# Performance work log

Hardware: AMD Instinct MI355X
Metric: run time of the kernel (lower is better)

## Reference

```python
import jax, jax.numpy as jnp
import numpy as np

B, S, V, E, H, O = 256, 128, 50000, 256, 512, 32


def _cell(x, h, c, Wih, Whh, bih, bhh):
    # PyTorch LSTM gate order: i, f, g, o
    g = x @ Wih.T + h @ Whh.T + bih + bhh
    i, f, gg, o = jnp.split(g, 4, axis=-1)
    c = jax.nn.sigmoid(f) * c + jax.nn.sigmoid(i) * jnp.tanh(gg)
    h = jax.nn.sigmoid(o) * jnp.tanh(c)
    return h, c


def setup_inputs() -> dict:
    key = jax.random.key(0)
    ks = iter(jax.random.split(key, 32))
    n = lambda shape: jax.random.normal(next(ks), shape, dtype=jnp.float32) * 0.05
    return {
        'x': jax.random.randint(next(ks), (B, S), 0, V),
        'emb': n((V, E)),
        'enc_Wih0': n((4 * H, E)), 'enc_Whh0': n((4 * H, H)),
        'enc_bih0': n((4 * H,)), 'enc_bhh0': n((4 * H,)),
        'enc_Wih1': n((4 * H, H)), 'enc_Whh1': n((4 * H, H)),
        'enc_bih1': n((4 * H,)), 'enc_bhh1': n((4 * H,)),
        'dec_Wih0': n((4 * H, O)), 'dec_Whh0': n((4 * H, H)),
        'dec_bih0': n((4 * H,)), 'dec_bhh0': n((4 * H,)),
        'dec_Wih1': n((4 * H, H)), 'dec_Whh1': n((4 * H, H)),
        'dec_bih1': n((4 * H,)), 'dec_bhh1': n((4 * H,)),
        'fc_w': n((S, O, H)), 'fc_b': n((S, O)),
    }


def reference(x, emb, enc_Wih0, enc_Whh0, enc_bih0, enc_bhh0,
              enc_Wih1, enc_Whh1, enc_bih1, enc_bhh1,
              dec_Wih0, dec_Whh0, dec_bih0, dec_bhh0,
              dec_Wih1, dec_Whh1, dec_bih1, dec_bhh1,
              fc_w, fc_b):
    b = x.shape[0]
    xe = jnp.swapaxes(emb[x], 0, 1)  # [S, B, E]
    z = jnp.zeros((b, H), jnp.float32)

    # 2-layer LSTM encoder (eval mode: no dropout)
    def enc0(carry, xi):
        h, c = _cell(xi, carry[0], carry[1], enc_Wih0, enc_Whh0, enc_bih0, enc_bhh0)
        return (h, c), h
    (h0, c0), y0 = jax.lax.scan(enc0, (z, z), xe)

    def enc1(carry, xi):
        h, c = _cell(xi, carry[0], carry[1], enc_Wih1, enc_Whh1, enc_bih1, enc_bhh1)
        return (h, c), h
    (h1, c1), _ = jax.lax.scan(enc1, (z, z), y0)

    # greedy decoder: one-hot of previous argmax fed back each step
    in0 = jnp.zeros((b, O), jnp.float32).at[:, 0].set(1.0)

    def dec(carry, wb):
        h0, c0, h1, c1, xin = carry
        w, bb = wb  # per-step Linear: w [O, H], bb [O]
        h0, c0 = _cell(xin, h0, c0, dec_Wih0, dec_Whh0, dec_bih0, dec_bhh0)
        h1, c1 = _cell(h0, h1, c1, dec_Wih1, dec_Whh1, dec_bih1, dec_bhh1)
        probs = jax.nn.softmax(h1 @ w.T + bb, axis=-1)  # [B, O]
        nxt = jax.nn.one_hot(jnp.argmax(probs, axis=-1), O, dtype=probs.dtype)
        return (h0, c0, h1, c1, nxt), probs

    _, out = jax.lax.scan(dec, (h0, c0, h1, c1, in0), (fc_w, fc_b))
    return jnp.swapaxes(out, 0, 1)  # [B, S, O]
```

## Files before the change

kernel.cpp:

```cpp
#include <hip/hip_runtime.h>


#define BN 256
#define SN 128
#define EN 256
#define HN 512
#define ON 32
#define RG 32
#define NCG 32
#define NTHREADS 256
#define XSTR 264
#define HSTR 520
#define GSTR 68
#define POLL_GUARD (1 << 20)

typedef _Float16 f16;
typedef _Float16 f16x8 __attribute__((ext_vector_type(8)));
typedef _Float16 f16x2 __attribute__((ext_vector_type(2)));
typedef float f32x4 __attribute__((ext_vector_type(4)));
typedef unsigned u32x4 __attribute__((ext_vector_type(4)));

__device__ __forceinline__ f32x4 MFMA16(f16x8 a, f16x8 b, f32x4 c) {
  return __builtin_amdgcn_mfma_f32_16x16x32_f16(a, b, c, 0, 0, 0);
}

__device__ __forceinline__ float sigf(float x) { return 1.0f / (1.0f + __expf(-x)); }

template<int NKT>
__device__ __forceinline__ void loadW(const float* __restrict__ Wb, int K, int col, int quad,
                                      f16x8* dst) {
  #pragma unroll
  for (int kt = 0; kt < NKT; ++kt) {
    const float* p = Wb + (size_t)col * K + kt * 32 + quad * 8;
    f32x4 a = *(const f32x4*)p;
    f32x4 b = *(const f32x4*)(p + 4);
    f16x8 h;
    h[0] = (f16)a[0]; h[1] = (f16)a[1]; h[2] = (f16)a[2]; h[3] = (f16)a[3];
    h[4] = (f16)b[0]; h[5] = (f16)b[1]; h[6] = (f16)b[2]; h[7] = (f16)b[3];
    dst[kt] = h;
  }
}

__device__ __forceinline__ void issue8(u32x4* v, const char* __restrict__ src, int tid) {
  const char* base = src + tid * 16;
  #pragma unroll
  for (int j = 0; j < 8; ++j)
    asm volatile("global_load_dwordx4 %0, %1, off sc1" : "=v"(v[j]) : "v"(base + j * 4096));
}
__device__ __forceinline__ void write8(f16* dst, const u32x4* v, int tid) {
  #pragma unroll
  for (int j = 0; j < 8; ++j) {
    int u = j * 256 + tid, rr = u >> 6, cc = u & 63;
    *(u32x4*)&dst[rr * HSTR + cc * 8] = v[j];
  }
}

template<int NKT>
__device__ __forceinline__ void matmulAcc(f32x4* acc, const f16* stage, int stride,
                                          const f16x8* Wr, int l16, int quad) {
  #pragma unroll
  for (int mt = 0; mt < 2; ++mt) {
    #pragma unroll
    for (int kt = 0; kt < NKT; ++kt) {
      f16x8 a = *(const f16x8*)&stage[(mt * 16 + l16) * stride + kt * 32 + quad * 8];
      acc[mt] = MFMA16(a, Wr[kt], acc[mt]);
    }
  }
}

__device__ __forceinline__ void barrier_arrive(int* slots, int g, int cg, int tid, int epoch) {
  __syncthreads();
  if (tid == 0) {
    asm volatile("s_waitcnt vmcnt(0)" ::: "memory");
    __hip_atomic_store(&slots[g * 64 + cg], epoch, __ATOMIC_RELAXED, __HIP_MEMORY_SCOPE_AGENT);
  }
}

__device__ __forceinline__ void barrier_wait(int* slots, int g, int tid, int epoch, int* esc) {
  if (!*esc) {
    int idx = tid & 31;
    int gd = 0;
    for (;;) {
      int v = __hip_atomic_load(&slots[g * 64 + idx], __ATOMIC_RELAXED, __HIP_MEMORY_SCOPE_AGENT);
      if (__all(v >= epoch)) break;
      if (++gd > POLL_GUARD) { *esc = 1; break; }
      __builtin_amdgcn_s_sleep(1);
    }
  }
  asm volatile("" ::: "memory");
}

__device__ __forceinline__ void gatherXE(f16* xes, const int* __restrict__ xTok,
                                         const float* __restrict__ emb, int g, int k, int tid) {
  int r = tid >> 3, sub = tid & 7;
  int tok = xTok[(g * RG + r) * SN + k];
  const float* er = emb + (size_t)tok * EN + sub * 32;
  f16* dst = &xes[r * XSTR + sub * 32];
  #pragma unroll
  for (int jj = 0; jj < 32; jj += 8) {
    f32x4 a = *(const f32x4*)(er + jj);
    f32x4 b = *(const f32x4*)(er + jj + 4);
    f16x8 hv;
    hv[0] = (f16)a[0]; hv[1] = (f16)a[1]; hv[2] = (f16)a[2]; hv[3] = (f16)a[3];
    hv[4] = (f16)b[0]; hv[5] = (f16)b[1]; hv[6] = (f16)b[2]; hv[7] = (f16)b[3];
    *(f16x8*)(dst + jj) = hv;
  }
}

__device__ __forceinline__ void pointwise_store(const float* gb, int row, int d0, float* cv,
                                                unsigned* __restrict__ hout, int g, int cg,
                                                int sub) {
  const float* gr = gb + row * GSTR + d0;
  union { unsigned u; f16x2 h; } hv;
  #pragma unroll
  for (int j = 0; j < 2; ++j) {
    float vi = gr[j], vf = gr[16 + j], vg = gr[32 + j], vo = gr[48 + j];
    cv[j] = sigf(vf) * cv[j] + sigf(vi) * tanhf(vg);
    hv.h[j] = (f16)(sigf(vo) * tanhf(cv[j]));
  }
  __hip_atomic_store(&hout[(g * RG + row) * 256 + cg * 8 + sub], hv.u,
                     __ATOMIC_RELAXED, __HIP_MEMORY_SCOPE_AGENT);
}

__launch_bounds__(NTHREADS, 1)
__global__ void lstm_all(const int* __restrict__ xTok, const float* __restrict__ emb,
    const float* __restrict__ eWih0, const float* __restrict__ eWhh0,
    const float* __restrict__ ebih0, const float* __restrict__ ebhh0,
    const float* __restrict__ eWih1, const float* __restrict__ eWhh1,
    const float* __restrict__ ebih1, const float* __restrict__ ebhh1,
    const float* __restrict__ dWih0, const float* __restrict__ dWhh0,
    const float* __restrict__ dbih0, const float* __restrict__ dbhh0,
    const float* __restrict__ dWih1, const float* __restrict__ dWhh1,
    const float* __restrict__ dbih1, const float* __restrict__ dbhh1,
    const float* __restrict__ fcw, const float* __restrict__ fcb,
    float* __restrict__ dout, char* __restrict__ h0buf, char* __restrict__ h1buf,
    int* __restrict__ slots)
{
  __shared__ __align__(16) char upool[RG * XSTR * 2];
  __shared__ __align__(16) f16 h0s[RG * HSTR];
  __shared__ __align__(16) f16 h1s[RG * HSTR];
  __shared__ float gbuf0[RG * GSTR];
  __shared__ float gbuf1[RG * GSTR];
  __shared__ int amaxlds[RG];
  __shared__ int esc;

  f16*   xes  = (f16*)upool;
  float* lbuf = (float*)upool;
  float* w0d  = (float*)(upool + 4352);

  const int tid  = threadIdx.x;
  const int g    = blockIdx.x & 7;
  const int cg   = blockIdx.x >> 3;
  const int w    = tid >> 6;
  const int lane = tid & 63;
  const int quad = lane >> 4;
  const int l16  = lane & 15;
  const int colg = w * HN + cg * 16 + l16;
  const int urow = tid >> 3;
  const int ud0  = (tid & 7) * 2;
  int epoch = 0;
  if (tid == 0) esc = 0;

  f16x8 Wi0r[8], Wh0r[16], Wi1r[16], Wh1r[16];
  loadW<8>(eWih0, EN, colg, quad, Wi0r);
  loadW<16>(eWhh0, HN, colg, quad, Wh0r);
  loadW<16>(eWih1, HN, colg, quad, Wi1r);
  loadW<16>(eWhh1, HN, colg, quad, Wh1r);
  float bias0 = ebih0[colg] + ebhh0[colg];
  float bias1 = ebih1[colg] + ebhh1[colg];

  gatherXE(xes, xTok, emb, g, 0, tid);
  float c0[2] = {0.f, 0.f}, c1[2] = {0.f, 0.f};
  {
    unsigned idx = (unsigned)(BN * 256 + (g * RG + urow) * 256 + cg * 8 + (tid & 7));
    __hip_atomic_store((unsigned*)h0buf + idx, 0u, __ATOMIC_RELAXED, __HIP_MEMORY_SCOPE_AGENT);
    __hip_atomic_store((unsigned*)h1buf + idx, 0u, __ATOMIC_RELAXED, __HIP_MEMORY_SCOPE_AGENT);
  }
  ++epoch; barrier_arrive(slots, g, cg, tid, epoch);
  __syncthreads();
  barrier_wait(slots, g, tid, epoch, &esc);

  for (int k = 0; k <= SN; ++k) {
    u32x4 v0[8], v1[8];
    issue8(v0, h0buf + (size_t)((k - 1) & 1) * BN * HN * 2 + (size_t)(g * RG) * HN * 2, tid);
    if (k >= 1)
      issue8(v1, h1buf + (size_t)(k & 1) * BN * HN * 2 + (size_t)(g * RG) * HN * 2, tid);

    f32x4 acc0[2], acc1[2];
    if (k < SN) {
      f32x4 b0; b0[0] = bias0; b0[1] = bias0; b0[2] = bias0; b0[3] = bias0;
      acc0[0] = b0; acc0[1] = b0;
      matmulAcc<8>(acc0, xes, XSTR, Wi0r, l16, quad);
    }
    if (k >= 1) asm volatile("s_waitcnt vmcnt(8)" ::: "memory");
    else        asm volatile("s_waitcnt vmcnt(0)" ::: "memory");
    write8(h0s, v0, tid);
    __syncthreads();
    if (k < SN) matmulAcc<16>(acc0, h0s, HSTR, Wh0r, l16, quad);
    if (k >= 1) {
      f32x4 b1; b1[0] = bias1; b1[1] = bias1; b1[2] = bias1; b1[3] = bias1;
      acc1[0] = b1; acc1[1] = b1;
      matmulAcc<16>(acc1, h0s, HSTR, Wi1r, l16, quad);
      asm volatile("s_waitcnt vmcnt(0)" ::: "memory");
      write8(h1s, v1, tid);
      __syncthreads();
      matmulAcc<16>(acc1, h1s, HSTR, Wh1r, l16, quad);
    }

    #pragma unroll
    for (int mt = 0; mt < 2; ++mt) {
      #pragma unroll
      for (int i = 0; i < 4; ++i) {
        int rr = (mt * 16 + quad * 4 + i) * GSTR + w * 16 + l16;
        if (k < SN) gbuf0[rr] = acc0[mt][i];
        if (k >= 1) gbuf1[rr] = acc1[mt][i];
      }
    }
    __syncthreads();
    if (k < SN)
      pointwise_store(gbuf0, urow, ud0, c0,
                      (unsigned*)(h0buf + (size_t)(k & 1) * BN * HN * 2), g, cg, tid & 7);
    if (k >= 1)
      pointwise_store(gbuf1, urow, ud0, c1,
                      (unsigned*)(h1buf + (size_t)((k - 1) & 1) * BN * HN * 2), g, cg, tid & 7);

    ++epoch;
    barrier_arrive(slots, g, cg, tid, epoch);
    if (k < SN - 1) gatherXE(xes, xTok, emb, g, k + 1, tid);
    __syncthreads();
    barrier_wait(slots, g, tid, epoch, &esc);
  }

  loadW<16>(dWhh0, HN, colg, quad, Wh0r);
  loadW<16>(dWih1, HN, colg, quad, Wi1r);
  loadW<16>(dWhh1, HN, colg, quad, Wh1r);
  bias0 = dbih0[colg] + dbhh0[colg];
  bias1 = dbih1[colg] + dbhh1[colg];
  {
    int cl = tid >> 2, i0 = (tid & 3) * 8;
    int gcol = (cl >> 4) * HN + cg * 16 + (cl & 15);
    const float* p = dWih0 + (size_t)gcol * ON + i0;
    #pragma unroll
    for (int j = 0; j < 8; ++j) w0d[cl * 32 + i0 + j] = p[j];
  }
  if (tid < RG) amaxlds[tid] = 0;

  for (int t = 0; t <= SN; ++t) {
    u32x4 v0[8];
    issue8(v0, h1buf + (size_t)((t - 1) & 1) * BN * HN * 2 + (size_t)(g * RG) * HN * 2, tid);

    f32x4 acc0[2];
    if (t < SN) {
      acc0[0] = f32x4{0.f, 0.f, 0.f, 0.f}; acc0[1] = acc0[0];
      matmulAcc<16>(acc0, h0s, HSTR, Wh0r, l16, quad);
    }
    asm volatile("s_waitcnt vmcnt(0)" ::: "memory");
    write8(h1s, v0, tid);
    __syncthreads();

    if (t >= 1) {
      int st = t - 1;
      int fmt = w & 1, fnt = w >> 1;
      int colo = fnt * 16 + l16;
      f32x4 afc;
      { float fb = fcb[st * ON + colo]; afc[0] = fb; afc[1] = fb; afc[2] = fb; afc[3] = fb; }
      #pragma unroll
      for (int kt = 0; kt < 16; ++kt) {
        const float* p = fcw + ((size_t)st * ON + colo) * HN + kt * 32 + quad * 8;
        f32x4 a = *(const f32x4*)p;
        f32x4 b = *(const f32x4*)(p + 4);
        f16x8 bf;
        bf[0] = (f16)a[0]; bf[1] = (f16)a[1]; bf[2] = (f16)a[2]; bf[3] = (f16)a[3];
        bf[4] = (f16)b[0]; bf[5] = (f16)b[1]; bf[6] = (f16)b[2]; bf[7] = (f16)b[3];
        f16x8 av = *(const f16x8*)&h1s[(fmt * 16 + l16) * HSTR + kt * 32 + quad * 8];
        afc = MFMA16(av, bf, afc);
      }
      #pragma unroll
      for (int i = 0; i < 4; ++i)
        lbuf[(fmt * 16 + quad * 4 + i) * 33 + colo] = afc[i];
      __syncthreads();
      {
        int row = tid >> 3, s = tid & 7, cbase = s * 4;
        float vv[4];
        #pragma unroll
        for (int j = 0; j < 4; ++j) vv[j] = lbuf[row * 33 + cbase + j];
        float mx = vv[0]; int bi = cbase;
        #pragma unroll
        for (int j = 1; j < 4; ++j)
          if (vv[j] > mx) { mx = vv[j]; bi = cbase + j; }
        #pragma unroll
        for (int m = 1; m < 8; m <<= 1) {
          float om = __shfl_xor(mx, m);
          int   ob = __shfl_xor(bi, m);
          if (om > mx || (om == mx && ob < bi)) { mx = om; bi = ob; }
        }
        float e[4], ss = 0.f;
        #pragma unroll
        for (int j = 0; j < 4; ++j) { e[j] = __expf(vv[j] - mx); ss += e[j]; }
        #pragma unroll
        for (int m = 1; m < 8; m <<= 1) ss += __shfl_xor(ss, m);
        if (s == 0) amaxlds[row] = bi;
        if (cg == 0) {
          float inv = 1.0f / ss;
          float* op = dout + ((size_t)(g * RG + row) * SN + st) * ON + cbase;
          #pragma unroll
          for (int j = 0; j < 4; ++j) op[j] = e[j] * inv;
        }
      }
      __syncthreads();
    }

    if (t < SN) {
      #pragma unroll
      for (int mt = 0; mt < 2; ++mt) {
        #pragma unroll
        for (int i = 0; i < 4; ++i) {
          int row = mt * 16 + quad * 4 + i;
          acc0[mt][i] += bias0 + w0d[(w * 16 + l16) * 32 + amaxlds[row]];
        }
      }
      #pragma unroll
      for (int mt = 0; mt < 2; ++mt) {
        #pragma unroll
        for (int i = 0; i < 4; ++i)
          gbuf0[(mt * 16 + quad * 4 + i) * GSTR + w * 16 + l16] = acc0[mt][i];
      }
      __syncthreads();
      pointwise_store(gbuf0, urow, ud0, c0,
                      (unsigned*)(h0buf + (size_t)(t & 1) * BN * HN * 2), g, cg, tid & 7);
    }
    ++epoch; barrier_arrive(slots, g, cg, tid, epoch); barrier_wait(slots, g, tid, epoch, &esc);

    if (t < SN) {
      u32x4 v2[8];
      issue8(v2, h0buf + (size_t)(t & 1) * BN * HN * 2 + (size_t)(g * RG) * HN * 2, tid);
      f32x4 acc1[2];
      f32x4 b1; b1[0] = bias1; b1[1] = bias1; b1[2] = bias1; b1[3] = bias1;
      acc1[0] = b1; acc1[1] = b1;
      matmulAcc<16>(acc1, h1s, HSTR, Wh1r, l16, quad);
      asm volatile("s_waitcnt vmcnt(0)" ::: "memory");
      write8(h0s, v2, tid);
      __syncthreads();
      matmulAcc<16>(acc1, h0s, HSTR, Wi1r, l16, quad);
      #pragma unroll
      for (int mt = 0; mt < 2; ++mt) {
        #pragma unroll
        for (int i = 0; i < 4; ++i)
          gbuf0[(mt * 16 + quad * 4 + i) * GSTR + w * 16 + l16] = acc1[mt][i];
      }
      __syncthreads();
      pointwise_store(gbuf0, urow, ud0, c1,
                      (unsigned*)(h1buf + (size_t)(t & 1) * BN * HN * 2), g, cg, tid & 7);
      ++epoch; barrier_arrive(slots, g, cg, tid, epoch); barrier_wait(slots, g, tid, epoch, &esc);
    }
  }
}

extern "C" void kernel_launch(void* const* d_in, const int* in_sizes, int n_in,
                              void* d_out, int out_size, void* d_ws, size_t ws_size,
                              hipStream_t stream) {
  (void)in_sizes; (void)n_in; (void)out_size; (void)ws_size;
  const int*   xTok  = (const int*)d_in[0];
  const float* emb   = (const float*)d_in[1];
  const float* eWih0 = (const float*)d_in[2];
  const float* eWhh0 = (const float*)d_in[3];
  const float* ebih0 = (const float*)d_in[4];
  const float* ebhh0 = (const float*)d_in[5];
  const float* eWih1 = (const float*)d_in[6];
  const float* eWhh1 = (const float*)d_in[7];
  const float* ebih1 = (const float*)d_in[8];
  const float* ebhh1 = (const float*)d_in[9];
  const float* dWih0 = (const float*)d_in[10];
  const float* dWhh0 = (const float*)d_in[11];
  const float* dbih0 = (const float*)d_in[12];
  const float* dbhh0 = (const float*)d_in[13];
  const float* dWih1 = (const float*)d_in[14];
  const float* dWhh1 = (const float*)d_in[15];
  const float* dbih1 = (const float*)d_in[16];
  const float* dbhh1 = (const float*)d_in[17];
  const float* fcw   = (const float*)d_in[18];
  const float* fcb   = (const float*)d_in[19];

  char* h0buf = (char*)d_ws;
  char* h1buf = (char*)d_ws + (size_t)2 * BN * HN * 2;
  int*  slots = (int*)((char*)d_ws + (size_t)4 * BN * HN * 2);

  hipLaunchKernelGGL(lstm_all, dim3(256), dim3(NTHREADS), 0, stream,
                     xTok, emb, eWih0, eWhh0, ebih0, ebhh0, eWih1, eWhh1, ebih1, ebhh1,
                     dWih0, dWhh0, dbih0, dbhh0, dWih1, dWhh1, dbih1, dbhh1,
                     fcw, fcb, (float*)d_out, h0buf, h1buf, slots);
}
```

Before: 3.006 ms.

## Use atomic-counter group barrier and prestage FC weights into LDS during barrier wait

Replaces the per-block epoch-slot barrier, where every wave polls 32 slots, with one atomic-add counter per group that blocks poll against a growing target. It also converts the per-step fc weight slice to fp16 and stages it in shared memory while waiting at the barrier, so the FC MFMA reads LDS instead of loading and converting fp32 from global memory on the critical path. The cost is extra LDS usage and contention on a single atomic counter. The counter reset relies on the initial slot handshake for ordering.

```diff
diff --git a/kernel.cpp b/kernel.cpp
--- a/kernel.cpp
+++ b/kernel.cpp
@@ -11,6 +11,7 @@
 #define NTHREADS 256
 #define XSTR 264
 #define HSTR 520
+#define FSTR 520
 #define GSTR 68
 #define POLL_GUARD (1 << 20)
 
@@ -68,21 +69,23 @@
   }
 }
 
-__device__ __forceinline__ void barrier_arrive(int* slots, int g, int cg, int tid, int epoch) {
+__device__ __forceinline__ void arrive_ctr(int* slots, int g, int tid) {
   __syncthreads();
   if (tid == 0) {
     asm volatile("s_waitcnt vmcnt(0)" ::: "memory");
-    __hip_atomic_store(&slots[g * 64 + cg], epoch, __ATOMIC_RELAXED, __HIP_MEMORY_SCOPE_AGENT);
-  }
-}
-
-__device__ __forceinline__ void barrier_wait(int* slots, int g, int tid, int epoch, int* esc) {
+    int one = 1;
+    int* p = &slots[g * 64 + 40];
+    asm volatile("global_atomic_add %0, %1, off" :: "v"(p), "v"(one) : "memory");
+  }
+}
+
+__device__ __forceinline__ void wait_ctr(int* slots, int g, int target, int* esc) {
   if (!*esc) {
-    int idx = tid & 31;
+    const int* p = &slots[g * 64 + 40];
     int gd = 0;
     for (;;) {
-      int v = __hip_atomic_load(&slots[g * 64 + idx], __ATOMIC_RELAXED, __HIP_MEMORY_SCOPE_AGENT);
-      if (__all(v >= epoch)) break;
+      int v = __hip_atomic_load(p, __ATOMIC_RELAXED, __HIP_MEMORY_SCOPE_AGENT);
+      if (v >= target) break;
       if (++gd > POLL_GUARD) { *esc = 1; break; }
       __builtin_amdgcn_s_sleep(1);
     }
@@ -104,6 +107,22 @@
     hv[0] = (f16)a[0]; hv[1] = (f16)a[1]; hv[2] = (f16)a[2]; hv[3] = (f16)a[3];
     hv[4] = (f16)b[0]; hv[5] = (f16)b[1]; hv[6] = (f16)b[2]; hv[7] = (f16)b[3];
     *(f16x8*)(dst + jj) = hv;
+  }
+}
+
+__device__ __forceinline__ void stageFCW(f16* fcwb, const float* __restrict__ fcw,
+                                         int st, int tid) {
+  int col = tid >> 3, k0 = (tid & 7) * 64;
+  const float* src = fcw + ((size_t)st * ON + col) * HN + k0;
+  f16* dstp = &fcwb[col * FSTR + k0];
+  #pragma unroll
+  for (int jj = 0; jj < 64; jj += 8) {
+    f32x4 a = *(const f32x4*)(src + jj);
+    f32x4 b = *(const f32x4*)(src + jj + 4);
+    f16x8 hv;
+    hv[0] = (f16)a[0]; hv[1] = (f16)a[1]; hv[2] = (f16)a[2]; hv[3] = (f16)a[3];
+    hv[4] = (f16)b[0]; hv[5] = (f16)b[1]; hv[6] = (f16)b[2]; hv[7] = (f16)b[3];
+    *(f16x8*)(dstp + jj) = hv;
   }
 }
 
@@ -139,6 +158,7 @@
   __shared__ __align__(16) char upool[RG * XSTR * 2];
   __shared__ __align__(16) f16 h0s[RG * HSTR];
   __shared__ __align__(16) f16 h1s[RG * HSTR];
+  __shared__ __align__(16) f16 fcwb[ON * FSTR];
   __shared__ float gbuf0[RG * GSTR];
   __shared__ float gbuf1[RG * GSTR];
   __shared__ int amaxlds[RG];
@@ -158,7 +178,7 @@
   const int colg = w * HN + cg * 16 + l16;
   const int urow = tid >> 3;
   const int ud0  = (tid & 7) * 2;
-  int epoch = 0;
+  int ctarget = 0;
   if (tid == 0) esc = 0;
 
   f16x8 Wi0r[8], Wh0r[16], Wi1r[16], Wh1r[16];
@@ -176,9 +196,23 @@
     __hip_atomic_store((unsigned*)h0buf + idx, 0u, __ATOMIC_RELAXED, __HIP_MEMORY_SCOPE_AGENT);
     __hip_atomic_store((unsigned*)h1buf + idx, 0u, __ATOMIC_RELAXED, __HIP_MEMORY_SCOPE_AGENT);
   }
-  ++epoch; barrier_arrive(slots, g, cg, tid, epoch);
   __syncthreads();
-  barrier_wait(slots, g, tid, epoch, &esc);
+  if (tid == 0) {
+    __hip_atomic_store(&slots[g * 64 + 40], 0, __ATOMIC_RELAXED, __HIP_MEMORY_SCOPE_AGENT);
+    asm volatile("s_waitcnt vmcnt(0)" ::: "memory");
+    __hip_atomic_store(&slots[g * 64 + cg], 1, __ATOMIC_RELAXED, __HIP_MEMORY_SCOPE_AGENT);
+  }
+  if (!esc) {
+    int idx = tid & 31;
+    int gd = 0;
+    for (;;) {
+      int v = __hip_atomic_load(&slots[g * 64 + idx], __ATOMIC_RELAXED, __HIP_MEMORY_SCOPE_AGENT);
+      if (__all(v >= 1)) break;
+      if (++gd > POLL_GUARD) { esc = 1; break; }
+      __builtin_amdgcn_s_sleep(1);
+    }
+  }
+  __syncthreads();
 
   for (int k = 0; k <= SN; ++k) {
     u32x4 v0[8], v1[8];
@@ -224,11 +258,11 @@
       pointwise_store(gbuf1, urow, ud0, c1,
                       (unsigned*)(h1buf + (size_t)((k - 1) & 1) * BN * HN * 2), g, cg, tid & 7);
 
-    ++epoch;
-    barrier_arrive(slots, g, cg, tid, epoch);
+    arrive_ctr(slots, g, tid);
     if (k < SN - 1) gatherXE(xes, xTok, emb, g, k + 1, tid);
     __syncthreads();
-    barrier_wait(slots, g, tid, epoch, &esc);
+    ctarget += NCG;
+    wait_ctr(slots, g, ctarget, &esc);
   }
 
   loadW<16>(dWhh0, HN, colg, quad, Wh0r);
@@ -248,6 +282,8 @@
   for (int t = 0; t <= SN; ++t) {
     u32x4 v0[8];
     issue8(v0, h1buf + (size_t)((t - 1) & 1) * BN * HN * 2 + (size_t)(g * RG) * HN * 2, tid);
+    float fb = 0.f;
+    if (t >= 1) fb = fcb[(t - 1) * ON + ((w >> 1) * 16 + l16)];
 
     f32x4 acc0[2];
     if (t < SN) {
@@ -259,27 +295,21 @@
     __syncthreads();
 
     if (t >= 1) {
-      int st = t - 1;
       int fmt = w & 1, fnt = w >> 1;
       int colo = fnt * 16 + l16;
-      f32x4 afc;
-      { float fb = fcb[st * ON + colo]; afc[0] = fb; afc[1] = fb; afc[2] = fb; afc[3] = fb; }
+      f32x4 afc = {0.f, 0.f, 0.f, 0.f};
       #pragma unroll
       for (int kt = 0; kt < 16; ++kt) {
-        const float* p = fcw + ((size_t)st * ON + colo) * HN + kt * 32 + quad * 8;
-        f32x4 a = *(const f32x4*)p;
-        f32x4 b = *(const f32x4*)(p + 4);
-        f16x8 bf;
-        bf[0] = (f16)a[0]; bf[1] = (f16)a[1]; bf[2] = (f16)a[2]; bf[3] = (f16)a[3];
-        bf[4] = (f16)b[0]; bf[5] = (f16)b[1]; bf[6] = (f16)b[2]; bf[7] = (f16)b[3];
+        f16x8 bf = *(const f16x8*)&fcwb[colo * FSTR + kt * 32 + quad * 8];
         f16x8 av = *(const f16x8*)&h1s[(fmt * 16 + l16) * HSTR + kt * 32 + quad * 8];
         afc = MFMA16(av, bf, afc);
       }
       #pragma unroll
       for (int i = 0; i < 4; ++i)
-        lbuf[(fmt * 16 + quad * 4 + i) * 33 + colo] = afc[i];
+        lbuf[(fmt * 16 + quad * 4 + i) * 33 + colo] = afc[i] + fb;
       __syncthreads();
       {
+        int st = t - 1;
         int row = tid >> 3, s = tid & 7, cbase = s * 4;
         float vv[4];
         #pragma unroll
@@ -329,7 +359,9 @@
       pointwise_store(gbuf0, urow, ud0, c0,
                       (unsigned*)(h0buf + (size_t)(t & 1) * BN * HN * 2), g, cg, tid & 7);
     }
-    ++epoch; barrier_arrive(slots, g, cg, tid, epoch); barrier_wait(slots, g, tid, epoch, &esc);
+    arrive_ctr(slots, g, tid);
+    ctarget += NCG;
+    wait_ctr(slots, g, ctarget, &esc);
 
     if (t < SN) {
       u32x4 v2[8];
@@ -351,7 +383,11 @@
       __syncthreads();
       pointwise_store(gbuf0, urow, ud0, c1,
                       (unsigned*)(h1buf + (size_t)(t & 1) * BN * HN * 2), g, cg, tid & 7);
-      ++epoch; barrier_arrive(slots, g, cg, tid, epoch); barrier_wait(slots, g, tid, epoch, &esc);
+      arrive_ctr(slots, g, tid);
+      stageFCW(fcwb, fcw, t, tid);
+      __syncthreads();
+      ctarget += NCG;
+      wait_ctr(slots, g, ctarget, &esc);
     }
   }
 }
```

New measurement: 2.413 ms. 1.25x faster.
